# Optimization experiments

Hardware: AMD Instinct MI355X
Metric: run time of the kernel (lower is better)

Reference implementation:

```python
import jax, jax.numpy as jnp
import numpy as np
from jax import lax

B, T, H = 512, 1024, 256
NUM_CLASSES = 9


def simple_rnn_last(x, W, U, b):
    """Keras SimpleRNN with tanh, return_sequences=False.
    x: [B,T,D], W: [D,H], U: [H,H], b: [H] -> last hidden [B,H]."""
    xW = jnp.einsum('btd,dh->bth', x, W) + b  # precompute input projection
    h0 = jnp.zeros((x.shape[0], U.shape[0]), x.dtype)

    def step(h, xw_t):
        h = jnp.tanh(xw_t + h @ U)
        return h, None

    hT, _ = lax.scan(step, h0, jnp.swapaxes(xW, 0, 1))  # scan over time [T,B,H]
    return hT


def setup_inputs() -> dict:
    key = jax.random.key(0)
    ks = jax.random.split(key, 16)
    g = lambda k, shp, fan: jax.random.normal(k, shp, jnp.float32) / np.sqrt(fan)
    return {
        'x':   jax.random.normal(ks[0], (B, T, 1), jnp.float32),
        'W1':  g(ks[1], (1, H), 1),
        'U1':  g(ks[2], (H, H), H),
        'b1':  jnp.zeros((H,), jnp.float32),
        'W2':  g(ks[3], (1, H), 1),
        'U2':  g(ks[4], (H, H), H),
        'b2':  jnp.zeros((H,), jnp.float32),
        'Wd1': g(ks[5], (H, 128), H),
        'bd1': jnp.zeros((128,), jnp.float32),
        'Wd2': g(ks[6], (128, 64), 128),
        'bd2': jnp.zeros((64,), jnp.float32),
        'Wd3': g(ks[7], (64, 32), 64),
        'bd3': jnp.zeros((32,), jnp.float32),
        'Wd4': g(ks[8], (32, NUM_CLASSES), 32),
        'bd4': jnp.zeros((NUM_CLASSES,), jnp.float32),
    }


def reference(x, W1, U1, b1, W2, U2, b2, Wd1, bd1, Wd2, bd2, Wd3, bd3, Wd4, bd4):
    h1 = simple_rnn_last(x, W1, U1, b1)            # [B,256]
    h2 = simple_rnn_last(h1[:, :, None], W2, U2, b2)  # treat 256 features as a sequence -> [B,256]
    z = jax.nn.relu(h2 @ Wd1 + bd1)                # dropout = identity at inference
    z = jax.nn.relu(z @ Wd2 + bd2)
    z = jax.nn.relu(z @ Wd3 + bd3)
    return z @ Wd4 + bd4                           # logits [B,num_classes]
```

## Files before the change

kernel.cpp:

```cpp
#include <hip/hip_runtime.h>
#include <math.h>

#define NCLS 9

typedef __attribute__((ext_vector_type(8))) short short8;
typedef __attribute__((ext_vector_type(4))) float f32x4;

__device__ __forceinline__ unsigned short f2bf(float f) {
    unsigned int u = __float_as_uint(f);
    return (unsigned short)((u + 0x7fffu + ((u >> 16) & 1u)) >> 16);
}

__device__ __forceinline__ short8 as_s8(uint4 v) {
    union { uint4 u; short8 s; } x; x.u = v; return x.s;
}

__device__ __forceinline__ float fast_tanh(float x) {
    float s = x * 2.885390081777927f;
    float e, r;
    asm("v_exp_f32 %0, %1" : "=v"(e) : "v"(s));
    asm("v_rcp_f32 %0, %1" : "=v"(r) : "v"(e + 1.0f));
    return fmaf(-2.0f, r, 1.0f);
}

__global__ __launch_bounds__(512, 2) void rnn_fused_kernel(
    const float* __restrict__ x,
    const float* __restrict__ W1, const float* __restrict__ U1, const float* __restrict__ b1,
    const float* __restrict__ W2, const float* __restrict__ U2, const float* __restrict__ b2,
    float* __restrict__ h2out)
{
    const int tid  = threadIdx.x;
    const int w    = tid >> 6;
    const int lane = tid & 63;
    const int g    = lane >> 4;
    const int l16  = lane & 15;
    const int b0   = blockIdx.x << 1;

    __shared__ uint4  hbuf[2][64];
    __shared__ float2 xall[1024];
    __shared__ float2 seq2[256];

    {
        const float4* x4 = (const float4*)x;
        const int row = tid >> 8, tq = tid & 255;
        const float4 v = x4[(b0 + row) * 256 + tq];
        ((float*)&xall[tq * 4 + 0])[row] = v.x;
        ((float*)&xall[tq * 4 + 1])[row] = v.y;
        ((float*)&xall[tq * 4 + 2])[row] = v.z;
        ((float*)&xall[tq * 4 + 3])[row] = v.w;
        ((unsigned int*)hbuf)[tid] = 0u;
    }

    int rd_off[8];
    #pragma unroll
    for (int kk = 0; kk < 8; ++kk)
        rd_off[kk] = (kk * 8 + g * 2 + (l16 & 1)) << 4;
    const int g2w = (l16 >> 2) & 3, s4 = l16 & 3;
    int wr_off[2];
    #pragma unroll
    for (int r = 0; r < 2; ++r)
        wr_off[r] = ((w * 8 + g2w * 2 + r) << 4) + 4 * s4;
    const int col0 = w * 32 + 2 * l16;
    char* const hbase = (char*)hbuf;

#pragma unroll 1
    for (int p = 0; p < 2; ++p) {
        const float* W    = p ? W2 : W1;
        const float* U    = p ? U2 : U1;
        const float* bias = p ? b2 : b1;
        const int    T    = p ? 256 : 1024;

        uint4 bfrag[2][8];
        #pragma unroll
        for (int t2 = 0; t2 < 2; ++t2) {
            #pragma unroll
            for (int kk = 0; kk < 8; ++kk) {
                unsigned int d[4];
                #pragma unroll
                for (int pr = 0; pr < 4; ++pr) {
                    const int k0 = kk * 32 + g * 8 + 2 * pr;
                    d[pr] = (unsigned)f2bf(U[k0 * 256 + col0 + t2])
                          | ((unsigned)f2bf(U[(k0 + 1) * 256 + col0 + t2]) << 16);
                }
                bfrag[t2][kk] = make_uint4(d[0], d[1], d[2], d[3]);
            }
        }
        #pragma unroll
        for (int t2 = 0; t2 < 2; ++t2)
            #pragma unroll
            for (int kk = 0; kk < 8; ++kk)
                asm volatile("" : "+v"(bfrag[t2][kk].x), "+v"(bfrag[t2][kk].y),
                                  "+v"(bfrag[t2][kk].z), "+v"(bfrag[t2][kk].w));

        const float2 wv2 = *(const float2*)&W[col0];
        const float2 bv2 = *(const float2*)&bias[col0];

        if (p == 1) {
            if (tid < 256) ((unsigned int*)hbuf)[tid] = 0u;
        }
        __syncthreads();

        float2 svc = p ? seq2[0] : xall[0];

        for (int t = 0; t < T; ++t) {
            char* const hcur = hbase + ((t & 1) << 10);
            char* const hnxt = hbase + (((t & 1) ^ 1) << 10);

            uint4 a[8];
            #pragma unroll
            for (int kk = 0; kk < 8; ++kk)
                a[kk] = *(const uint4*)(hcur + rd_off[kk]);

            f32x4 aA0, aA1;
            f32x4 aB0 = {0.f, 0.f, 0.f, 0.f}, aB1 = {0.f, 0.f, 0.f, 0.f};
            aA0[0] = fmaf(svc.x, wv2.x, bv2.x);
            aA0[1] = fmaf(svc.y, wv2.x, bv2.x);
            aA0[2] = aA0[0]; aA0[3] = aA0[1];
            aA1[0] = fmaf(svc.x, wv2.y, bv2.y);
            aA1[1] = fmaf(svc.y, wv2.y, bv2.y);
            aA1[2] = aA1[0]; aA1[3] = aA1[1];

            #pragma unroll
            for (int kp = 0; kp < 4; ++kp) {
                aA0 = __builtin_amdgcn_mfma_f32_16x16x32_bf16(
                    as_s8(a[2 * kp]), as_s8(bfrag[0][2 * kp]), aA0, 0, 0, 0);
                aA1 = __builtin_amdgcn_mfma_f32_16x16x32_bf16(
                    as_s8(a[2 * kp]), as_s8(bfrag[1][2 * kp]), aA1, 0, 0, 0);
                aB0 = __builtin_amdgcn_mfma_f32_16x16x32_bf16(
                    as_s8(a[2 * kp + 1]), as_s8(bfrag[0][2 * kp + 1]), aB0, 0, 0, 0);
                aB1 = __builtin_amdgcn_mfma_f32_16x16x32_bf16(
                    as_s8(a[2 * kp + 1]), as_s8(bfrag[1][2 * kp + 1]), aB1, 0, 0, 0);
            }

            {
                const int tn = (t + 1 < T) ? t + 1 : 0;
                svc = p ? seq2[tn] : xall[tn];
            }

            const float h00 = fast_tanh(aA0[0] + aB0[0]);
            const float h01 = fast_tanh(aA0[1] + aB0[1]);
            const float h10 = fast_tanh(aA1[0] + aB1[0]);
            const float h11 = fast_tanh(aA1[1] + aB1[1]);
            unsigned pk0, pk1;
            asm("v_cvt_pk_bf16_f32 %0, %1, %2" : "=v"(pk0) : "v"(h00), "v"(h10));
            asm("v_cvt_pk_bf16_f32 %0, %1, %2" : "=v"(pk1) : "v"(h01), "v"(h11));

            if (g == 0) {
                *(unsigned int*)(hnxt + wr_off[0]) = pk0;
                *(unsigned int*)(hnxt + wr_off[1]) = pk1;
                if (t == T - 1) {
                    if (p == 0) {
                        seq2[col0]     = make_float2(h00, h01);
                        seq2[col0 + 1] = make_float2(h10, h11);
                    } else {
                        *(float2*)&h2out[(b0 + 0) * 256 + col0] = make_float2(h00, h10);
                        *(float2*)&h2out[(b0 + 1) * 256 + col0] = make_float2(h01, h11);
                    }
                }
            }
            __syncthreads();
        }
    }
}

__global__ __launch_bounds__(128) void mlp_kernel(
    const float* __restrict__ h2,
    const float* __restrict__ Wd1, const float* __restrict__ bd1,
    const float* __restrict__ Wd2, const float* __restrict__ bd2,
    const float* __restrict__ Wd3, const float* __restrict__ bd3,
    const float* __restrict__ Wd4, const float* __restrict__ bd4,
    float* __restrict__ out)
{
    const int b   = blockIdx.x;
    const int tid = threadIdx.x;

    __shared__ float hin[256];
    __shared__ float z1[128];
    __shared__ float z2[64];
    __shared__ float z3[32];

    hin[tid]       = h2[b * 256 + tid];
    hin[tid + 128] = h2[b * 256 + tid + 128];
    __syncthreads();

    {
        float a = bd1[tid];
#pragma unroll 8
        for (int i = 0; i < 256; ++i) a += hin[i] * Wd1[i * 128 + tid];
        z1[tid] = fmaxf(a, 0.0f);
    }
    __syncthreads();
    if (tid < 64) {
        float a = bd2[tid];
#pragma unroll 8
        for (int i = 0; i < 128; ++i) a += z1[i] * Wd2[i * 64 + tid];
        z2[tid] = fmaxf(a, 0.0f);
    }
    __syncthreads();
    if (tid < 32) {
        float a = bd3[tid];
#pragma unroll 8
        for (int i = 0; i < 64; ++i) a += z2[i] * Wd3[i * 32 + tid];
        z3[tid] = fmaxf(a, 0.0f);
    }
    __syncthreads();
    if (tid < NCLS) {
        float a = bd4[tid];
#pragma unroll
        for (int i = 0; i < 32; ++i) a += z3[i] * Wd4[i * NCLS + tid];
        out[b * NCLS + tid] = a;
    }
}

extern "C" void kernel_launch(void* const* d_in, const int* in_sizes, int n_in,
                              void* d_out, int out_size, void* d_ws, size_t ws_size,
                              hipStream_t stream) {
    const float* x   = (const float*)d_in[0];
    const float* W1  = (const float*)d_in[1];
    const float* U1  = (const float*)d_in[2];
    const float* b1  = (const float*)d_in[3];
    const float* W2  = (const float*)d_in[4];
    const float* U2  = (const float*)d_in[5];
    const float* b2  = (const float*)d_in[6];
    const float* Wd1 = (const float*)d_in[7];
    const float* bd1 = (const float*)d_in[8];
    const float* Wd2 = (const float*)d_in[9];
    const float* bd2 = (const float*)d_in[10];
    const float* Wd3 = (const float*)d_in[11];
    const float* bd3 = (const float*)d_in[12];
    const float* Wd4 = (const float*)d_in[13];
    const float* bd4 = (const float*)d_in[14];

    float* out = (float*)d_out;
    float* h2  = (float*)d_ws;

    rnn_fused_kernel<<<256, 512, 0, stream>>>(x, W1, U1, b1, W2, U2, b2, h2);
    mlp_kernel<<<512, 128, 0, stream>>>(h2, Wd1, bd1, Wd2, bd2, Wd3, bd3, Wd4, bd4, out);
}
```

Before: 596.0 us.

## Split recurrent matmul K dimension across wave pairs with LDS partial-sum reduction

Reorganizes the 8 waves into 4 column groups by 2 K-halves. Each wave loads half the hidden-state fragments and covers 64 columns, and the upper-half waves pass partial sums through shared memory to the lower-half waves, which apply tanh and write the next state. This shortens the per-accumulator MFMA dependency chain and the LDS read volume per wave. In exchange it adds an extra block barrier and an LDS round trip on every timestep of the serial recurrence.

```diff
diff --git a/kernel.cpp b/kernel.cpp
--- a/kernel.cpp
+++ b/kernel.cpp
@@ -34,11 +34,14 @@
     const int lane = tid & 63;
     const int g    = lane >> 4;
     const int l16  = lane & 15;
+    const int wp   = w & 3;
+    const int hi   = w >> 2;
     const int b0   = blockIdx.x << 1;
 
     __shared__ uint4  hbuf[2][64];
     __shared__ float2 xall[1024];
     __shared__ float2 seq2[256];
+    __shared__ float4 pbuf[4][2][16];
 
     {
         const float4* x4 = (const float4*)x;
@@ -51,16 +54,17 @@
         ((unsigned int*)hbuf)[tid] = 0u;
     }
 
-    int rd_off[8];
+    int rd_off[4];
     #pragma unroll
-    for (int kk = 0; kk < 8; ++kk)
-        rd_off[kk] = (kk * 8 + g * 2 + (l16 & 1)) << 4;
-    const int g2w = (l16 >> 2) & 3, s4 = l16 & 3;
-    int wr_off[2];
+    for (int kkl = 0; kkl < 4; ++kkl)
+        rd_off[kkl] = (((hi * 4 + kkl) * 8) + g * 2 + (l16 & 1)) << 4;
+    int wr_off[2][2];
     #pragma unroll
-    for (int r = 0; r < 2; ++r)
-        wr_off[r] = ((w * 8 + g2w * 2 + r) << 4) + 4 * s4;
-    const int col0 = w * 32 + 2 * l16;
+    for (int u = 0; u < 2; ++u)
+        #pragma unroll
+        for (int m = 0; m < 2; ++m)
+            wr_off[u][m] = (((2 * wp + u) * 8 + ((2 * l16 >> 3) & 3) * 2 + m) << 4)
+                         + 4 * (l16 & 3);
     char* const hbase = (char*)hbuf;
 
 #pragma unroll 1
@@ -70,30 +74,38 @@
         const float* bias = p ? b2 : b1;
         const int    T    = p ? 256 : 1024;
 
-        uint4 bfrag[2][8];
+        uint4 bfrag[2][2][4];
         #pragma unroll
-        for (int t2 = 0; t2 < 2; ++t2) {
-            #pragma unroll
-            for (int kk = 0; kk < 8; ++kk) {
-                unsigned int d[4];
-                #pragma unroll
-                for (int pr = 0; pr < 4; ++pr) {
-                    const int k0 = kk * 32 + g * 8 + 2 * pr;
-                    d[pr] = (unsigned)f2bf(U[k0 * 256 + col0 + t2])
-                          | ((unsigned)f2bf(U[(k0 + 1) * 256 + col0 + t2]) << 16);
-                }
-                bfrag[t2][kk] = make_uint4(d[0], d[1], d[2], d[3]);
+        for (int u = 0; u < 2; ++u) {
+            #pragma unroll
+            for (int v = 0; v < 2; ++v) {
+                const int col = wp * 64 + u * 32 + 2 * l16 + v;
+                #pragma unroll
+                for (int kkl = 0; kkl < 4; ++kkl) {
+                    unsigned int d[4];
+                    #pragma unroll
+                    for (int pr = 0; pr < 4; ++pr) {
+                        const int k0 = (hi * 4 + kkl) * 32 + g * 8 + 2 * pr;
+                        d[pr] = (unsigned)f2bf(U[k0 * 256 + col])
+                              | ((unsigned)f2bf(U[(k0 + 1) * 256 + col]) << 16);
+                    }
+                    bfrag[u][v][kkl] = make_uint4(d[0], d[1], d[2], d[3]);
+                }
             }
         }
         #pragma unroll
-        for (int t2 = 0; t2 < 2; ++t2)
-            #pragma unroll
-            for (int kk = 0; kk < 8; ++kk)
-                asm volatile("" : "+v"(bfrag[t2][kk].x), "+v"(bfrag[t2][kk].y),
-                                  "+v"(bfrag[t2][kk].z), "+v"(bfrag[t2][kk].w));
-
-        const float2 wv2 = *(const float2*)&W[col0];
-        const float2 bv2 = *(const float2*)&bias[col0];
+        for (int u = 0; u < 2; ++u)
+            #pragma unroll
+            for (int v = 0; v < 2; ++v)
+                #pragma unroll
+                for (int kkl = 0; kkl < 4; ++kkl)
+                    asm volatile("" : "+v"(bfrag[u][v][kkl].x), "+v"(bfrag[u][v][kkl].y),
+                                      "+v"(bfrag[u][v][kkl].z), "+v"(bfrag[u][v][kkl].w));
+
+        const float2 wv[2] = { *(const float2*)&W[wp * 64 + 2 * l16],
+                               *(const float2*)&W[wp * 64 + 32 + 2 * l16] };
+        const float2 bv[2] = { *(const float2*)&bias[wp * 64 + 2 * l16],
+                               *(const float2*)&bias[wp * 64 + 32 + 2 * l16] };
 
         if (p == 1) {
             if (tid < 256) ((unsigned int*)hbuf)[tid] = 0u;
@@ -106,55 +118,90 @@
             char* const hcur = hbase + ((t & 1) << 10);
             char* const hnxt = hbase + (((t & 1) ^ 1) << 10);
 
-            uint4 a[8];
-            #pragma unroll
-            for (int kk = 0; kk < 8; ++kk)
-                a[kk] = *(const uint4*)(hcur + rd_off[kk]);
-
-            f32x4 aA0, aA1;
-            f32x4 aB0 = {0.f, 0.f, 0.f, 0.f}, aB1 = {0.f, 0.f, 0.f, 0.f};
-            aA0[0] = fmaf(svc.x, wv2.x, bv2.x);
-            aA0[1] = fmaf(svc.y, wv2.x, bv2.x);
-            aA0[2] = aA0[0]; aA0[3] = aA0[1];
-            aA1[0] = fmaf(svc.x, wv2.y, bv2.y);
-            aA1[1] = fmaf(svc.y, wv2.y, bv2.y);
-            aA1[2] = aA1[0]; aA1[3] = aA1[1];
-
-            #pragma unroll
-            for (int kp = 0; kp < 4; ++kp) {
-                aA0 = __builtin_amdgcn_mfma_f32_16x16x32_bf16(
-                    as_s8(a[2 * kp]), as_s8(bfrag[0][2 * kp]), aA0, 0, 0, 0);
-                aA1 = __builtin_amdgcn_mfma_f32_16x16x32_bf16(
-                    as_s8(a[2 * kp]), as_s8(bfrag[1][2 * kp]), aA1, 0, 0, 0);
-                aB0 = __builtin_amdgcn_mfma_f32_16x16x32_bf16(
-                    as_s8(a[2 * kp + 1]), as_s8(bfrag[0][2 * kp + 1]), aB0, 0, 0, 0);
-                aB1 = __builtin_amdgcn_mfma_f32_16x16x32_bf16(
-                    as_s8(a[2 * kp + 1]), as_s8(bfrag[1][2 * kp + 1]), aB1, 0, 0, 0);
+            uint4 a[4];
+            #pragma unroll
+            for (int kkl = 0; kkl < 4; ++kkl)
+                a[kkl] = *(const uint4*)(hcur + rd_off[kkl]);
+
+            f32x4 acc[2][2];
+            if (hi == 0) {
+                #pragma unroll
+                for (int u = 0; u < 2; ++u) {
+                    acc[u][0][0] = fmaf(svc.x, wv[u].x, bv[u].x);
+                    acc[u][0][1] = fmaf(svc.y, wv[u].x, bv[u].x);
+                    acc[u][0][2] = acc[u][0][0]; acc[u][0][3] = acc[u][0][1];
+                    acc[u][1][0] = fmaf(svc.x, wv[u].y, bv[u].y);
+                    acc[u][1][1] = fmaf(svc.y, wv[u].y, bv[u].y);
+                    acc[u][1][2] = acc[u][1][0]; acc[u][1][3] = acc[u][1][1];
+                }
+            } else {
+                #pragma unroll
+                for (int u = 0; u < 2; ++u)
+                    #pragma unroll
+                    for (int v = 0; v < 2; ++v)
+                        acc[u][v] = (f32x4){0.f, 0.f, 0.f, 0.f};
+            }
+
+            #pragma unroll
+            for (int kkl = 0; kkl < 4; ++kkl) {
+                #pragma unroll
+                for (int u = 0; u < 2; ++u)
+                    #pragma unroll
+                    for (int v = 0; v < 2; ++v)
+                        acc[u][v] = __builtin_amdgcn_mfma_f32_16x16x32_bf16(
+                            as_s8(a[kkl]), as_s8(bfrag[u][v][kkl]), acc[u][v], 0, 0, 0);
+            }
+
+            if (hi && g == 0) {
+                pbuf[wp][0][l16] = make_float4(acc[0][0][0], acc[0][0][1],
+                                               acc[0][1][0], acc[0][1][1]);
+                pbuf[wp][1][l16] = make_float4(acc[1][0][0], acc[1][0][1],
+                                               acc[1][1][0], acc[1][1][1]);
             }
 
             {
                 const int tn = (t + 1 < T) ? t + 1 : 0;
                 svc = p ? seq2[tn] : xall[tn];
             }
-
-            const float h00 = fast_tanh(aA0[0] + aB0[0]);
-            const float h01 = fast_tanh(aA0[1] + aB0[1]);
-            const float h10 = fast_tanh(aA1[0] + aB1[0]);
-            const float h11 = fast_tanh(aA1[1] + aB1[1]);
-            unsigned pk0, pk1;
-            asm("v_cvt_pk_bf16_f32 %0, %1, %2" : "=v"(pk0) : "v"(h00), "v"(h10));
-            asm("v_cvt_pk_bf16_f32 %0, %1, %2" : "=v"(pk1) : "v"(h01), "v"(h11));
-
-            if (g == 0) {
-                *(unsigned int*)(hnxt + wr_off[0]) = pk0;
-                *(unsigned int*)(hnxt + wr_off[1]) = pk1;
-                if (t == T - 1) {
-                    if (p == 0) {
-                        seq2[col0]     = make_float2(h00, h01);
-                        seq2[col0 + 1] = make_float2(h10, h11);
-                    } else {
-                        *(float2*)&h2out[(b0 + 0) * 256 + col0] = make_float2(h00, h10);
-                        *(float2*)&h2out[(b0 + 1) * 256 + col0] = make_float2(h01, h11);
+            __syncthreads();
+
+            if (hi == 0) {
+                float h[2][2][2];
+                #pragma unroll
+                for (int u = 0; u < 2; ++u) {
+                    const float4 pp = pbuf[wp][u][l16];
+                    h[u][0][0] = fast_tanh(acc[u][0][0] + pp.x);
+                    h[u][0][1] = fast_tanh(acc[u][0][1] + pp.y);
+                    h[u][1][0] = fast_tanh(acc[u][1][0] + pp.z);
+                    h[u][1][1] = fast_tanh(acc[u][1][1] + pp.w);
+                }
+                unsigned pk[2][2];
+                #pragma unroll
+                for (int u = 0; u < 2; ++u)
+                    #pragma unroll
+                    for (int m = 0; m < 2; ++m)
+                        asm("v_cvt_pk_bf16_f32 %0, %1, %2"
+                            : "=v"(pk[u][m]) : "v"(h[u][0][m]), "v"(h[u][1][m]));
+                if (g == 0) {
+                    #pragma unroll
+                    for (int u = 0; u < 2; ++u) {
+                        *(unsigned int*)(hnxt + wr_off[u][0]) = pk[u][0];
+                        *(unsigned int*)(hnxt + wr_off[u][1]) = pk[u][1];
+                    }
+                    if (t == T - 1) {
+                        #pragma unroll
+                        for (int u = 0; u < 2; ++u) {
+                            const int colb = wp * 64 + u * 32 + 2 * l16;
+                            if (p == 0) {
+                                seq2[colb]     = make_float2(h[u][0][0], h[u][0][1]);
+                                seq2[colb + 1] = make_float2(h[u][1][0], h[u][1][1]);
+                            } else {
+                                *(float2*)&h2out[(b0 + 0) * 256 + colb] =
+                                    make_float2(h[u][0][0], h[u][1][0]);
+                                *(float2*)&h2out[(b0 + 1) * 256 + colb] =
+                                    make_float2(h[u][0][1], h[u][1][1]);
+                            }
+                        }
                     }
                 }
             }
```

New measurement: 866.5 us. 1.45x slower.
